# Kernel optimization log

Measured on AMD Instinct MI355X. Metric: run time of the kernel, lower is better.

The kernel has to match this reference:

```python
import jax, jax.numpy as jnp
import numpy as np
from jax import lax

LEAK = 0.9            # leaking_rate alpha
SPECTRAL = 0.9
DENSITY = 0.9
B, S, N, F_IN, H, L = 8, 128, 64, 32, 256, 3


def _make_whh(rng, h):
    w = rng.uniform(-1.0, 1.0, size=(h, h)).astype(np.float32)
    mask = rng.uniform(size=(h, h)) < DENSITY
    w = w * mask
    rho = np.max(np.abs(np.linalg.eigvals(w)))
    return (w * (SPECTRAL / rho)).astype(np.float32)


def setup_inputs() -> dict:
    key = jax.random.key(0)
    kx, = jax.random.split(key, 1)
    rng = np.random.default_rng(0)
    x = jax.random.normal(kx, (B, S, N, F_IN), dtype=jnp.float32)
    w_ih0 = jnp.asarray(rng.uniform(-1.0, 1.0, size=(H, F_IN)).astype(np.float32))
    w_ih = jnp.asarray(rng.uniform(-1.0, 1.0, size=(L - 1, H, H)).astype(np.float32))
    b_ih = jnp.asarray(rng.uniform(-1.0, 1.0, size=(L, H)).astype(np.float32))
    w_hh = jnp.stack([jnp.asarray(_make_whh(rng, H)) for _ in range(L)])
    return {"x": x, "w_ih0": w_ih0, "w_ih": w_ih, "b_ih": b_ih,
            "w_hh": w_hh, "time_scale": 1}


def _run_layer(x_in, w_i, b_i, w_h):
    # x_in: [b,s,n,f]; leaky-integrator ESN layer.
    u = jnp.einsum('bsnf,hf->bsnh', x_in, w_i) + b_i          # input drive
    h0 = jnp.zeros((x_in.shape[0], x_in.shape[2], w_h.shape[0]), x_in.dtype)

    def step(h, u_t):
        h_new = (1.0 - LEAK) * h + LEAK * jnp.tanh(
            u_t + jnp.einsum('bnh,gh->bng', h, w_h))
        return h_new, h_new

    _, hs = lax.scan(step, h0, jnp.moveaxis(u, 1, 0))         # [s,b,n,h]
    return jnp.moveaxis(hs, 0, 1)                             # [b,s,n,h]


def reference(x, w_ih0, w_ih, b_ih, w_hh, time_scale):
    states = []
    inp = x
    for l in range(L):
        w_i = w_ih0 if l == 0 else w_ih[l - 1]
        inp = _run_layer(inp, w_i, b_ih[l], w_hh[l])
        states.append(inp)
    ox = jnp.concatenate(states, axis=-1)                     # [b,s,n,L*H]
    b, s, n, lf = ox.shape
    f = lf // time_scale
    return ox.reshape(b, s, n, time_scale, f)
```

## Files before the change

### kernel.cpp

```cpp
#include <hip/hip_runtime.h>
#include <cstdint>
#include <cstddef>

typedef _Float16 f16;
typedef _Float16 half8 __attribute__((ext_vector_type(8)));
typedef _Float16 half4 __attribute__((ext_vector_type(4)));
typedef float float4v __attribute__((ext_vector_type(4)));

static __device__ __forceinline__ float4v mfma16(half8 a, half8 b, float4v c) {
  return __builtin_amdgcn_mfma_f32_16x16x32_f16(a, b, c, 0, 0, 0);
}


__global__ __launch_bounds__(256, 2) void gemm_u(
    const float* __restrict__ A, int ldA, int K,
    const float* __restrict__ W,
    const float* __restrict__ bias,
    float* __restrict__ outp, int outcol)
{
  __shared__ alignas(16) f16 Ah[4096];
  __shared__ alignas(16) f16 Al[4096];
  __shared__ alignas(16) f16 Bh[8192];
  __shared__ alignas(16) f16 Bl[8192];

  const int tid = threadIdx.x;
  const int w = tid >> 6, lane = tid & 63, q = lane >> 4, c = lane & 15;
  const int mbase = blockIdx.x * 128;
  const int seg = tid & 7, rbase = tid >> 3;

  float4v acc[2][16] = {};
  const int nchunk = K >> 5;

  float4v va[4], vb[8];
  #pragma unroll
  for (int it = 0; it < 4; ++it)
    va[it] = *(const float4v*)(A + (size_t)(mbase + it * 32 + rbase) * ldA + seg * 4);
  #pragma unroll
  for (int it = 0; it < 8; ++it)
    vb[it] = *(const float4v*)(W + (size_t)(it * 32 + rbase) * K + seg * 4);

  for (int kc = 0; kc < nchunk; ++kc) {
    #pragma unroll
    for (int it = 0; it < 4; ++it) {
      int row = it * 32 + rbase;
      float4v v = va[it];
      f16 h0 = (f16)v.x, h1 = (f16)v.y, h2 = (f16)v.z, h3 = (f16)v.w;
      half4 hi = {h0, h1, h2, h3};
      half4 lo = {(f16)(v.x - (float)h0), (f16)(v.y - (float)h1),
                  (f16)(v.z - (float)h2), (f16)(v.w - (float)h3)};
      int mt = row >> 4, m = row & 15, qq = seg >> 1, jj = (seg & 1) * 4;
      int ofs = ((mt * 4 + qq) * 16 + m) * 8 + jj;
      *(half4*)&Ah[ofs] = hi;
      *(half4*)&Al[ofs] = lo;
    }
    #pragma unroll
    for (int it = 0; it < 8; ++it) {
      int g = it * 32 + rbase;
      float4v v = vb[it];
      f16 h0 = (f16)v.x, h1 = (f16)v.y, h2 = (f16)v.z, h3 = (f16)v.w;
      half4 hi = {h0, h1, h2, h3};
      half4 lo = {(f16)(v.x - (float)h0), (f16)(v.y - (float)h1),
                  (f16)(v.z - (float)h2), (f16)(v.w - (float)h3)};
      int nt = g >> 4, n = g & 15, qq = seg >> 1, jj = (seg & 1) * 4;
      int ofs = ((nt * 4 + qq) * 16 + n) * 8 + jj;
      *(half4*)&Bh[ofs] = hi;
      *(half4*)&Bl[ofs] = lo;
    }
    __syncthreads();

    if (kc + 1 < nchunk) {
      int ko = (kc + 1) * 32;
      #pragma unroll
      for (int it = 0; it < 4; ++it)
        va[it] = *(const float4v*)(A + (size_t)(mbase + it * 32 + rbase) * ldA + ko + seg * 4);
      #pragma unroll
      for (int it = 0; it < 8; ++it)
        vb[it] = *(const float4v*)(W + (size_t)(it * 32 + rbase) * K + ko + seg * 4);
    }

    half8 ah[2], al[2];
    #pragma unroll
    for (int m2 = 0; m2 < 2; ++m2) {
      int mt = w * 2 + m2;
      int ofs = ((mt * 4 + q) * 16 + c) * 8;
      ah[m2] = *(half8*)&Ah[ofs];
      al[m2] = *(half8*)&Al[ofs];
    }
    #pragma unroll
    for (int nt = 0; nt < 16; ++nt) {
      int ofs = ((nt * 4 + q) * 16 + c) * 8;
      half8 bh = *(half8*)&Bh[ofs];
      half8 bl = *(half8*)&Bl[ofs];
      #pragma unroll
      for (int m2 = 0; m2 < 2; ++m2) {
        acc[m2][nt] = mfma16(ah[m2], bh, acc[m2][nt]);
        acc[m2][nt] = mfma16(al[m2], bh, acc[m2][nt]);
        acc[m2][nt] = mfma16(ah[m2], bl, acc[m2][nt]);
      }
    }
    __syncthreads();
  }

  #pragma unroll
  for (int m2 = 0; m2 < 2; ++m2) {
    const int m2t = w * 2 + m2;
    const int b_ = mbase >> 13;
    const int t_ = ((mbase >> 6) + (m2t >> 2)) & 127;
    const int n0 = (m2t & 3) * 16;
    const size_t rowbase =
        ((size_t)b_ * 8192 + (size_t)((t_ + 1) & 127) * 64 + n0) * 768
        + outcol + (q * 16 + c) * 4;
    #pragma unroll
    for (int nt = 0; nt < 16; ++nt) {
      const float bsv = bias[nt * 16 + c];
      float4v vst;
      vst.x = acc[m2][nt][0] + bsv;
      vst.y = acc[m2][nt][1] + bsv;
      vst.z = acc[m2][nt][2] + bsv;
      vst.w = acc[m2][nt][3] + bsv;
      *(float4v*)&outp[rowbase + (size_t)nt * 768] = vst;
    }
  }
}

__global__ __launch_bounds__(1024, 1) void rec_layer(
    float* __restrict__ io, const float* __restrict__ whh, int outcol)
{
  __shared__ alignas(16) f16 hbuf[2][4096];

  const int tid = threadIdx.x;
  const int w = tid >> 6, lane = tid & 63, q = lane >> 4, c = lane & 15;
  const int r0 = blockIdx.x * 16;
  const int b_ = r0 >> 6, n0 = r0 & 63;

  half8 wf[8];
  {
    const int g = w * 16 + c;
    #pragma unroll
    for (int kc = 0; kc < 8; ++kc) {
      const float* src = whh + (size_t)g * 256 + kc * 32 + q * 8;
      float4v v0 = *(const float4v*)src;
      float4v v1 = *(const float4v*)(src + 4);
      half8 h = {(f16)v0.x, (f16)v0.y, (f16)v0.z, (f16)v0.w,
                 (f16)v1.x, (f16)v1.y, (f16)v1.z, (f16)v1.w};
      wf[kc] = h;
    }
  }

  {
    uint32_t* p = (uint32_t*)hbuf;
    #pragma unroll
    for (int i = 0; i < 4; ++i) p[tid + i * 1024] = 0u;
  }

  float hreg[4] = {};
  size_t base[4];
  #pragma unroll
  for (int i = 0; i < 4; ++i) {
    const int r = r0 + q * 4 + i;
    base[i] = ((size_t)(r >> 6) * 8192 + (r & 63)) * 768 + outcol + w * 16 + c;
  }

  const size_t ucell0 =
      ((size_t)b_ * 8192 + n0 + w) * 768 + outcol + (q * 16 + c) * 4;

  float4v uv127, uvc;
  uv127 = *(const float4v*)&io[ucell0];
  uvc   = *(const float4v*)&io[ucell0 + 49152];

  __syncthreads();

  for (int t = 0; t < 128; ++t) {
    const f16* rb = hbuf[t & 1];
    f16* wb = hbuf[(t + 1) & 1];

    half8 af[8];
    #pragma unroll
    for (int kc = 0; kc < 8; ++kc)
      af[kc] = *(const half8*)&rb[((kc * 4 + q) * 16 + c) * 8];

    float4v uvn;
    if (t < 126)
      uvn = *(const float4v*)&io[ucell0 + (size_t)(t + 2) * 49152];

    float4v acc0 = uvc;
    float4v acc1 = (float4v){0.f, 0.f, 0.f, 0.f};
    #pragma unroll
    for (int kc = 0; kc < 4; ++kc) {
      acc0 = mfma16(af[kc], wf[kc], acc0);
      acc1 = mfma16(af[kc + 4], wf[kc + 4], acc1);
    }

    const size_t sofs = (size_t)t * 49152;
    const int gcol = w * 16 + c;
    const int widx = (((gcol >> 5) * 4 + ((gcol >> 3) & 3)) * 16) * 8 + (gcol & 7);
    #pragma unroll
    for (int i = 0; i < 4; ++i) {
      const float xv = acc0[i] + acc1[i];
      const float e  = __builtin_amdgcn_exp2f(xv * 2.8853900817779268f);
      const float rr = __builtin_amdgcn_rcpf(e + 1.0f);
      const float hn = fmaf(-1.8f, rr, fmaf(0.1f, hreg[i], 0.9f));
      hreg[i] = hn;
      io[base[i] + sofs] = hn;
      wb[widx + (q * 4 + i) * 8] = (f16)hn;
    }

    if (t < 127) {
      asm volatile("s_waitcnt lgkmcnt(0)\n\ts_barrier" ::: "memory");
      uvc = (t == 126) ? uv127 : uvn;
    }
  }
}

extern "C" void kernel_launch(void* const* d_in, const int* in_sizes, int n_in,
                              void* d_out, int out_size, void* d_ws, size_t ws_size,
                              hipStream_t stream) {
  (void)in_sizes; (void)n_in; (void)out_size; (void)d_ws; (void)ws_size;
  const float* x     = (const float*)d_in[0];
  const float* w_ih0 = (const float*)d_in[1];
  const float* w_ih  = (const float*)d_in[2];
  const float* b_ih  = (const float*)d_in[3];
  const float* w_hh  = (const float*)d_in[4];
  float* out = (float*)d_out;

  gemm_u<<<512, 256, 0, stream>>>(x,         32,  32, w_ih0,         b_ih,       out, 0);
  rec_layer<<<32, 1024, 0, stream>>>(out, w_hh,            0);
  gemm_u<<<512, 256, 0, stream>>>(out,       768, 256, w_ih,          b_ih + 256, out, 256);
  rec_layer<<<32, 1024, 0, stream>>>(out, w_hh + 65536,    256);
  gemm_u<<<512, 256, 0, stream>>>(out + 256, 768, 256, w_ih + 65536,  b_ih + 512, out, 512);
  rec_layer<<<32, 1024, 0, stream>>>(out, w_hh + 131072,   512);
}
```

Baseline: 532.2 us.

## Pre-split input weights to fp16 hi/lo once and stream into LDS directly

```diff
diff --git a/kernel.cpp b/kernel.cpp
--- a/kernel.cpp
+++ b/kernel.cpp
@@ -11,6 +11,28 @@
   return __builtin_amdgcn_mfma_f32_16x16x32_f16(a, b, c, 0, 0, 0);
 }
 
+static __device__ __forceinline__ void gload_lds16(const void* g, void* l) {
+  __builtin_amdgcn_global_load_lds(
+      (const __attribute__((address_space(1))) void*)g,
+      (__attribute__((address_space(3))) void*)l, 16, 0, 0);
+}
+
+
+__global__ __launch_bounds__(256) void prep_w(
+    const float* __restrict__ w_ih, f16* __restrict__ wsf)
+{
+  const int idx = blockIdx.x * 256 + threadIdx.x;
+  const int l = idx >> 16, e = idx & 65535;
+  const int g = e >> 8, k = e & 255;
+  const float v = w_ih[(size_t)l * 65536 + e];
+  const f16 hi = (f16)v;
+  const f16 lo = (f16)(v - (float)hi);
+  const int kc = k >> 5, qq = (k >> 3) & 3, j = k & 7;
+  const int nt = g >> 4, n = g & 15;
+  const int fofs = kc * 8192 + ((nt * 4 + qq) * 16 + n) * 8 + j;
+  wsf[(size_t)l * 131072 + fofs] = hi;
+  wsf[(size_t)l * 131072 + 65536 + fofs] = lo;
+}
 
 __global__ __launch_bounds__(256, 2) void gemm_u(
     const float* __restrict__ A, int ldA, int K,
@@ -123,6 +145,104 @@
   }
 }
 
+__global__ __launch_bounds__(256, 2) void gemm_u_pw(
+    const float* __restrict__ A, int ldA,
+    const f16* __restrict__ Wf,
+    const float* __restrict__ bias,
+    float* __restrict__ outp, int outcol)
+{
+  __shared__ alignas(16) f16 Ah[4096];
+  __shared__ alignas(16) f16 Al[4096];
+  __shared__ alignas(16) f16 Bh[8192];
+  __shared__ alignas(16) f16 Bl[8192];
+
+  const int tid = threadIdx.x;
+  const int w = tid >> 6, lane = tid & 63, q = lane >> 4, c = lane & 15;
+  const int mbase = blockIdx.x * 128;
+  const int seg = tid & 7, rbase = tid >> 3;
+
+  float4v acc[2][16] = {};
+
+  float4v va[4];
+  #pragma unroll
+  for (int it = 0; it < 4; ++it)
+    va[it] = *(const float4v*)(A + (size_t)(mbase + it * 32 + rbase) * ldA + seg * 4);
+
+  for (int kc = 0; kc < 8; ++kc) {
+    #pragma unroll
+    for (int r = 0; r < 4; ++r) {
+      const int fo = kc * 8192 + (w * 4 + r) * 512;
+      gload_lds16(Wf + fo + lane * 8,          &Bh[(w * 4 + r) * 512]);
+      gload_lds16(Wf + 65536 + fo + lane * 8,  &Bl[(w * 4 + r) * 512]);
+    }
+
+    #pragma unroll
+    for (int it = 0; it < 4; ++it) {
+      int row = it * 32 + rbase;
+      float4v v = va[it];
+      f16 h0 = (f16)v.x, h1 = (f16)v.y, h2 = (f16)v.z, h3 = (f16)v.w;
+      half4 hi = {h0, h1, h2, h3};
+      half4 lo = {(f16)(v.x - (float)h0), (f16)(v.y - (float)h1),
+                  (f16)(v.z - (float)h2), (f16)(v.w - (float)h3)};
+      int mt = row >> 4, m = row & 15, qq = seg >> 1, jj = (seg & 1) * 4;
+      int ofs = ((mt * 4 + qq) * 16 + m) * 8 + jj;
+      *(half4*)&Ah[ofs] = hi;
+      *(half4*)&Al[ofs] = lo;
+    }
+    __syncthreads();
+
+    if (kc + 1 < 8) {
+      int ko = (kc + 1) * 32;
+      #pragma unroll
+      for (int it = 0; it < 4; ++it)
+        va[it] = *(const float4v*)(A + (size_t)(mbase + it * 32 + rbase) * ldA + ko + seg * 4);
+    }
+
+    half8 ah[2], al[2];
+    #pragma unroll
+    for (int m2 = 0; m2 < 2; ++m2) {
+      int mt = w * 2 + m2;
+      int ofs = ((mt * 4 + q) * 16 + c) * 8;
+      ah[m2] = *(half8*)&Ah[ofs];
+      al[m2] = *(half8*)&Al[ofs];
+    }
+    #pragma unroll
+    for (int nt = 0; nt < 16; ++nt) {
+      int ofs = ((nt * 4 + q) * 16 + c) * 8;
+      half8 bh = *(half8*)&Bh[ofs];
+      half8 bl = *(half8*)&Bl[ofs];
+      #pragma unroll
+      for (int m2 = 0; m2 < 2; ++m2) {
+        acc[m2][nt] = mfma16(ah[m2], bh, acc[m2][nt]);
+        acc[m2][nt] = mfma16(al[m2], bh, acc[m2][nt]);
+        acc[m2][nt] = mfma16(ah[m2], bl, acc[m2][nt]);
+      }
+    }
+    __syncthreads();
+  }
+
+  #pragma unroll
+  for (int m2 = 0; m2 < 2; ++m2) {
+    const int m2t = w * 2 + m2;
+    const int b_ = mbase >> 13;
+    const int t_ = ((mbase >> 6) + (m2t >> 2)) & 127;
+    const int n0 = (m2t & 3) * 16;
+    const size_t rowbase =
+        ((size_t)b_ * 8192 + (size_t)((t_ + 1) & 127) * 64 + n0) * 768
+        + outcol + (q * 16 + c) * 4;
+    #pragma unroll
+    for (int nt = 0; nt < 16; ++nt) {
+      const float bsv = bias[nt * 16 + c];
+      float4v vst;
+      vst.x = acc[m2][nt][0] + bsv;
+      vst.y = acc[m2][nt][1] + bsv;
+      vst.z = acc[m2][nt][2] + bsv;
+      vst.w = acc[m2][nt][3] + bsv;
+      *(float4v*)&outp[rowbase + (size_t)nt * 768] = vst;
+    }
+  }
+}
+
 __global__ __launch_bounds__(1024, 1) void rec_layer(
     float* __restrict__ io, const float* __restrict__ whh, int outcol)
 {
@@ -132,19 +252,16 @@
   const int w = tid >> 6, lane = tid & 63, q = lane >> 4, c = lane & 15;
   const int r0 = blockIdx.x * 16;
   const int b_ = r0 >> 6, n0 = r0 & 63;
+  const int gcol = w * 16 + c;
 
   half8 wf[8];
-  {
-    const int g = w * 16 + c;
-    #pragma unroll
-    for (int kc = 0; kc < 8; ++kc) {
-      const float* src = whh + (size_t)g * 256 + kc * 32 + q * 8;
-      float4v v0 = *(const float4v*)src;
-      float4v v1 = *(const float4v*)(src + 4);
-      half8 h = {(f16)v0.x, (f16)v0.y, (f16)v0.z, (f16)v0.w,
-                 (f16)v1.x, (f16)v1.y, (f16)v1.z, (f16)v1.w};
-      wf[kc] = h;
-    }
+  #pragma unroll
+  for (int kc = 0; kc < 8; ++kc) {
+    const float* src = whh + (size_t)gcol * 256 + kc * 32 + q * 8;
+    float4v v0 = *(const float4v*)src;
+    float4v v1 = *(const float4v*)(src + 4);
+    wf[kc] = (half8){(f16)v0.x, (f16)v0.y, (f16)v0.z, (f16)v0.w,
+                     (f16)v1.x, (f16)v1.y, (f16)v1.z, (f16)v1.w};
   }
 
   {
@@ -158,7 +275,7 @@
   #pragma unroll
   for (int i = 0; i < 4; ++i) {
     const int r = r0 + q * 4 + i;
-    base[i] = ((size_t)(r >> 6) * 8192 + (r & 63)) * 768 + outcol + w * 16 + c;
+    base[i] = ((size_t)(r >> 6) * 8192 + (r & 63)) * 768 + outcol + gcol;
   }
 
   const size_t ucell0 =
@@ -168,6 +285,8 @@
   uv127 = *(const float4v*)&io[ucell0];
   uvc   = *(const float4v*)&io[ucell0 + 49152];
 
+  const int widx = (((gcol >> 5) * 4 + ((gcol >> 3) & 3)) * 16) * 8 + (gcol & 7);
+
   __syncthreads();
 
   for (int t = 0; t < 128; ++t) {
@@ -192,8 +311,6 @@
     }
 
     const size_t sofs = (size_t)t * 49152;
-    const int gcol = w * 16 + c;
-    const int widx = (((gcol >> 5) * 4 + ((gcol >> 3) & 3)) * 16) * 8 + (gcol & 7);
     #pragma unroll
     for (int i = 0; i < 4; ++i) {
       const float xv = acc0[i] + acc1[i];
@@ -215,7 +332,7 @@
 extern "C" void kernel_launch(void* const* d_in, const int* in_sizes, int n_in,
                               void* d_out, int out_size, void* d_ws, size_t ws_size,
                               hipStream_t stream) {
-  (void)in_sizes; (void)n_in; (void)out_size; (void)d_ws; (void)ws_size;
+  (void)in_sizes; (void)n_in; (void)out_size;
   const float* x     = (const float*)d_in[0];
   const float* w_ih0 = (const float*)d_in[1];
   const float* w_ih  = (const float*)d_in[2];
@@ -223,10 +340,21 @@
   const float* w_hh  = (const float*)d_in[4];
   float* out = (float*)d_out;
 
-  gemm_u<<<512, 256, 0, stream>>>(x,         32,  32, w_ih0,         b_ih,       out, 0);
-  rec_layer<<<32, 1024, 0, stream>>>(out, w_hh,            0);
-  gemm_u<<<512, 256, 0, stream>>>(out,       768, 256, w_ih,          b_ih + 256, out, 256);
-  rec_layer<<<32, 1024, 0, stream>>>(out, w_hh + 65536,    256);
-  gemm_u<<<512, 256, 0, stream>>>(out + 256, 768, 256, w_ih + 65536,  b_ih + 512, out, 512);
-  rec_layer<<<32, 1024, 0, stream>>>(out, w_hh + 131072,   512);
-}
+  if (ws_size >= 2u * 131072u * sizeof(f16)) {
+    f16* wsf = (f16*)d_ws;
+    prep_w<<<512, 256, 0, stream>>>(w_ih, wsf);
+    gemm_u<<<512, 256, 0, stream>>>(x, 32, 32, w_ih0, b_ih, out, 0);
+    rec_layer<<<32, 1024, 0, stream>>>(out, w_hh, 0);
+    gemm_u_pw<<<512, 256, 0, stream>>>(out, 768, wsf, b_ih + 256, out, 256);
+    rec_layer<<<32, 1024, 0, stream>>>(out, w_hh + 65536, 256);
+    gemm_u_pw<<<512, 256, 0, stream>>>(out + 256, 768, wsf + 131072, b_ih + 512, out, 512);
+    rec_layer<<<32, 1024, 0, stream>>>(out, w_hh + 131072, 512);
+  } else {
+    gemm_u<<<512, 256, 0, stream>>>(x, 32, 32, w_ih0, b_ih, out, 0);
+    rec_layer<<<32, 1024, 0, stream>>>(out, w_hh, 0);
+    gemm_u<<<512, 256, 0, stream>>>(out, 768, 256, w_ih, b_ih + 256, out, 256);
+    rec_layer<<<32, 1024, 0, stream>>>(out, w_hh + 65536, 256);
+    gemm_u<<<512, 256, 0, stream>>>(out + 256, 768, 256, w_ih + 65536, b_ih + 512, out, 512);
+    rec_layer<<<32, 1024, 0, stream>>>(out, w_hh + 131072, 512);
+  }
+}
```

New measurement: 529.1 us. Within noise of the previous version (-0.6%).
